# Kernel tuning notes

Hardware: AMD Instinct MI355X
Metric: run time of the kernel (lower is better)

## Reference

```python
import jax, jax.numpy as jnp
import numpy as np


def _make_poly_power_deg1_d3():
    # monomials of degree<=1 in 3 vars: 1, x, y, z  (matches make_monomial_power(3,1))
    return jnp.array([[0, 0, 0], [1, 0, 0], [0, 1, 0], [0, 0, 1]], dtype=jnp.int32)


def setup_inputs() -> dict:
    key = jax.random.key(0)
    k1, k2, k3, k4 = jax.random.split(key, 4)
    Q, N, D, C = 32768, 1024, 3, 32
    q_pos = jax.random.normal(k1, (Q, D), dtype=jnp.float32)
    data_pos = jax.random.normal(k2, (N, D), dtype=jnp.float32)
    w = jax.random.normal(k3, (N, C), dtype=jnp.float32)
    c = jax.random.normal(k4, (4, C), dtype=jnp.float32)
    poly_power = _make_poly_power_deg1_d3()
    return {"q_pos": q_pos, "data_pos": data_pos, "w": w, "c": c, "poly_power": poly_power}


def reference(q_pos, data_pos, w, c, poly_power):
    # pairwise distance: [Q, N, D] -> [Q, N]
    diff = q_pos[:, None, :] - data_pos[None, :, :]
    r = jnp.sqrt(jnp.sum(diff * diff, axis=-1))
    # gaussian RBF kernel
    q_kernel_dist = jnp.exp(-(r * r))
    # interior=True: row-normalize kernel weights
    q_kernel_dist = q_kernel_dist / jnp.sum(q_kernel_dist, axis=-1, keepdims=True)
    # kernel-weighted sum of RBF coefficients: [N,C] x [Q,N] -> [Q,C]
    w_val = jnp.einsum('nc,qn->qc', w, q_kernel_dist)
    # polynomial basis values: prod over D of q_pos^power -> [Q, P]
    pp = poly_power.astype(q_pos.dtype)
    q_poly_val = jnp.prod(q_pos[:, None, :] ** pp[None, :, :], axis=-1)
    # poly-weighted sum: [P,C] x [Q,P] -> [Q,C]
    c_val = jnp.einsum('pc,qp->qc', c, q_poly_val)
    return (w_val + c_val, q_kernel_dist, q_poly_val)
```

## Files before the change

### kernel.cpp

```cpp
#include <hip/hip_runtime.h>
#include <hip/hip_bf16.h>

typedef __attribute__((ext_vector_type(8))) short short8;
typedef __attribute__((ext_vector_type(4))) float f32x4;

#define L2E 1.44269504088896340736f

__device__ __forceinline__ float ipow(float x, int e) {
    float r = 1.f;
    for (int i = 0; i < e; ++i) r *= x;
    return r;
}

__global__ __launch_bounds__(256, 2)
void rbf_fused(const float* __restrict__ q_pos,
               const float* __restrict__ data_pos,
               const float* __restrict__ w,
               const float* __restrict__ cmat,
               const int* __restrict__ poly_power,
               float* __restrict__ out_val,
               float* __restrict__ out_kd,
               float* __restrict__ out_poly)
{
    __shared__ __align__(16) unsigned char smem[65536 + 8192 + 768];
    unsigned char* const w_lds = smem;
    unsigned char* const a_lds = smem + 65536;
    float* const q_lds = (float*)(smem + 65536 + 8192);

    const int t  = threadIdx.x;
    const int l  = t & 63;
    const int wv = t >> 6;
    const int q0 = blockIdx.x * 64;

    for (int j = 0; j < 128; ++j) {
        int i = t + 256 * j;
        int n = i >> 5, cc = i & 31;
        __hip_bfloat16 h = __float2bfloat16(w[i]);
        *(__hip_bfloat16*)(w_lds + cc * 2048 + ((2 * n) ^ ((cc & 7) << 4))) = h;
    }
    if (t < 192) q_lds[t] = q_pos[q0 * 3 + t];
    {
        int i = blockIdx.x * 256 + t;
        int q = i >> 2, p = i & 3;
        int e0 = poly_power[p * 3 + 0], e1 = poly_power[p * 3 + 1], e2 = poly_power[p * 3 + 2];
        float x = q_pos[q * 3 + 0], y = q_pos[q * 3 + 1], z = q_pos[q * 3 + 2];
        out_poly[i] = ipow(x, e0) * ipow(y, e1) * ipow(z, e2);
    }
    __syncthreads();

    float qx[16], qy[16], qz[16];
#pragma unroll
    for (int r = 0; r < 16; ++r) {
        int row = wv * 16 + r;
        qx[r] = q_lds[row * 3 + 0];
        qy[r] = q_lds[row * 3 + 1];
        qz[r] = q_lds[row * 3 + 2];
    }

    float sum[16];
#pragma unroll
    for (int r = 0; r < 16; ++r) sum[r] = 0.f;
    for (int it = 0; it < 16; ++it) {
        int n = it * 64 + l;
        float px = data_pos[n * 3 + 0];
        float py = data_pos[n * 3 + 1];
        float pz = data_pos[n * 3 + 2];
#pragma unroll
        for (int r = 0; r < 16; ++r) {
            float dx = qx[r] - px, dy = qy[r] - py, dz = qz[r] - pz;
            float r2 = dx * dx + dy * dy + dz * dz;
            sum[r] += __builtin_amdgcn_exp2f(r2 * (-L2E));
        }
    }
    float inv[16];
#pragma unroll
    for (int r = 0; r < 16; ++r) {
        float s = sum[r];
        s += __shfl_xor(s, 1);  s += __shfl_xor(s, 2);  s += __shfl_xor(s, 4);
        s += __shfl_xor(s, 8);  s += __shfl_xor(s, 16); s += __shfl_xor(s, 32);
        inv[r] = 1.0f / s;
    }

    f32x4 acc0 = {0.f, 0.f, 0.f, 0.f};
    f32x4 acc1 = {0.f, 0.f, 0.f, 0.f};

    const int arow = l & 15;
    const int kq   = l >> 4;
    const int aswz = (arow & 7) << 4;
    unsigned char* const aw = a_lds + wv * 2048;
    const int offA0 = arow * 128 + (((0 * 32 + 8 * kq) * 2) ^ aswz);
    const int offA1 = arow * 128 + (((1 * 32 + 8 * kq) * 2) ^ aswz);
    const int c0   = arow;
    const int bswz = (c0 & 7) << 4;

    for (int ch = 0; ch < 16; ++ch) {
        int nb = ch * 64;
        int n = nb + l;
        float px = data_pos[n * 3 + 0];
        float py = data_pos[n * 3 + 1];
        float pz = data_pos[n * 3 + 2];
#pragma unroll
        for (int r = 0; r < 16; ++r) {
            float dx = qx[r] - px, dy = qy[r] - py, dz = qz[r] - pz;
            float r2 = dx * dx + dy * dy + dz * dz;
            float e  = __builtin_amdgcn_exp2f(r2 * (-L2E));
            float v  = e * inv[r];
            out_kd[(size_t)(q0 + wv * 16 + r) * 1024 + n] = v;
            *(__hip_bfloat16*)(aw + r * 128 + ((2 * l) ^ ((r & 7) << 4))) = __float2bfloat16(v);
        }
#pragma unroll
        for (int kk = 0; kk < 2; ++kk) {
            short8 afrag = *(const short8*)(aw + (kk ? offA1 : offA0));
            int n0 = nb + kk * 32 + 8 * kq;
            int boff = c0 * 2048 + ((2 * n0) ^ bswz);
            short8 b0 = *(const short8*)(w_lds + boff);
            short8 b1 = *(const short8*)(w_lds + boff + 16 * 2048);
            acc0 = __builtin_amdgcn_mfma_f32_16x16x32_bf16(afrag, b0, acc0, 0, 0, 0);
            acc1 = __builtin_amdgcn_mfma_f32_16x16x32_bf16(afrag, b1, acc1, 0, 0, 0);
        }
    }

    float cp0[4], cp1[4];
#pragma unroll
    for (int p = 0; p < 4; ++p) {
        cp0[p] = cmat[p * 32 + c0];
        cp1[p] = cmat[p * 32 + 16 + c0];
    }
    int pw[12];
#pragma unroll
    for (int i = 0; i < 12; ++i) pw[i] = poly_power[i];
#pragma unroll
    for (int r = 0; r < 4; ++r) {
        int row = kq * 4 + r;
        float x = q_lds[(wv * 16 + row) * 3 + 0];
        float y = q_lds[(wv * 16 + row) * 3 + 1];
        float z = q_lds[(wv * 16 + row) * 3 + 2];
        float cv0 = 0.f, cv1 = 0.f;
#pragma unroll
        for (int p = 0; p < 4; ++p) {
            float pv = ipow(x, pw[p * 3]) * ipow(y, pw[p * 3 + 1]) * ipow(z, pw[p * 3 + 2]);
            cv0 += cp0[p] * pv;
            cv1 += cp1[p] * pv;
        }
        int q = q0 + wv * 16 + row;
        out_val[q * 32 + c0]      = acc0[r] + cv0;
        out_val[q * 32 + 16 + c0] = acc1[r] + cv1;
    }
}

extern "C" void kernel_launch(void* const* d_in, const int* in_sizes, int n_in,
                              void* d_out, int out_size, void* d_ws, size_t ws_size,
                              hipStream_t stream) {
    const float* q_pos      = (const float*)d_in[0];
    const float* data_pos   = (const float*)d_in[1];
    const float* w          = (const float*)d_in[2];
    const float* cmat       = (const float*)d_in[3];
    const int*   poly_power = (const int*)d_in[4];

    const int Q = in_sizes[0] / 3;
    float* out      = (float*)d_out;
    float* out_val  = out;
    float* out_kd   = out + (size_t)Q * 32;
    float* out_poly = out_kd + (size_t)Q * 1024;

    int blocks = Q / 64;
    rbf_fused<<<blocks, 256, 0, stream>>>(q_pos, data_pos, w, cmat, poly_power,
                                          out_val, out_kd, out_poly);
}
```

Measured before the change: 169.8 us.

## Pre-pack w into MFMA fragment layout and compute A fragments in registers

A separate prep kernel converts w to bf16 once, stored in the exact MFMA B-fragment order in workspace, so the main kernel no longer stages 64KB of w in LDS per block. The main kernel now has each lane compute its own 8 kernel values directly into the A-fragment registers and write out_kd with float4 stores. The N dimension is split across two waves per 16-row group, with partial sums and accumulators combined through small shared arrays. This cuts LDS use, raises occupancy, and removes per-element LDS round trips. The cost is an extra kernel launch and some redundant data_pos loads.

```diff
diff --git a/kernel.cpp b/kernel.cpp
--- a/kernel.cpp
+++ b/kernel.cpp
@@ -12,139 +12,147 @@
     return r;
 }
 
-__global__ __launch_bounds__(256, 2)
-void rbf_fused(const float* __restrict__ q_pos,
-               const float* __restrict__ data_pos,
-               const float* __restrict__ w,
-               const float* __restrict__ cmat,
-               const int* __restrict__ poly_power,
-               float* __restrict__ out_val,
-               float* __restrict__ out_kd,
-               float* __restrict__ out_poly)
+__global__ void prep_w(const float* __restrict__ w, unsigned short* __restrict__ img)
 {
-    __shared__ __align__(16) unsigned char smem[65536 + 8192 + 768];
-    unsigned char* const w_lds = smem;
-    unsigned char* const a_lds = smem + 65536;
-    float* const q_lds = (float*)(smem + 65536 + 8192);
+    int idx = blockIdx.x * 256 + threadIdx.x;
+    int frag = idx >> 9, l = (idx >> 3) & 63, j = idx & 7;
+    int ct = frag & 1, kk = (frag >> 1) & 1, chg = frag >> 2;
+    int n = chg * 64 + kk * 32 + 8 * (l >> 4) + j;
+    int c = ct * 16 + (l & 15);
+    __hip_bfloat16 h = __float2bfloat16(w[n * 32 + c]);
+    img[idx] = *(unsigned short*)&h;
+}
 
+__global__ __launch_bounds__(256, 4)
+void rbf_main(const float* __restrict__ q_pos,
+              const float* __restrict__ data_pos,
+              const float* __restrict__ cmat,
+              const int* __restrict__ poly_power,
+              const unsigned short* __restrict__ wimg,
+              float* __restrict__ out_val,
+              float* __restrict__ out_kd,
+              float* __restrict__ out_poly)
+{
     const int t  = threadIdx.x;
     const int l  = t & 63;
     const int wv = t >> 6;
-    const int q0 = blockIdx.x * 64;
+    const int rg   = wv >> 1;
+    const int half = wv & 1;
+    const int q0 = blockIdx.x * 32 + rg * 16;
+    const int m  = l & 15;
+    const int kq = l >> 4;
 
-    for (int j = 0; j < 128; ++j) {
-        int i = t + 256 * j;
-        int n = i >> 5, cc = i & 31;
-        __hip_bfloat16 h = __float2bfloat16(w[i]);
-        *(__hip_bfloat16*)(w_lds + cc * 2048 + ((2 * n) ^ ((cc & 7) << 4))) = h;
-    }
-    if (t < 192) q_lds[t] = q_pos[q0 * 3 + t];
-    {
-        int i = blockIdx.x * 256 + t;
-        int q = i >> 2, p = i & 3;
-        int e0 = poly_power[p * 3 + 0], e1 = poly_power[p * 3 + 1], e2 = poly_power[p * 3 + 2];
-        float x = q_pos[q * 3 + 0], y = q_pos[q * 3 + 1], z = q_pos[q * 3 + 2];
-        out_poly[i] = ipow(x, e0) * ipow(y, e1) * ipow(z, e2);
-    }
-    __syncthreads();
+    __shared__ float s_sum[2][2][16];
+    __shared__ float s_acc[2][64][8];
 
-    float qx[16], qy[16], qz[16];
-#pragma unroll
-    for (int r = 0; r < 16; ++r) {
-        int row = wv * 16 + r;
-        qx[r] = q_lds[row * 3 + 0];
-        qy[r] = q_lds[row * 3 + 1];
-        qz[r] = q_lds[row * 3 + 2];
+    const float qx = q_pos[(q0 + m) * 3 + 0];
+    const float qy = q_pos[(q0 + m) * 3 + 1];
+    const float qz = q_pos[(q0 + m) * 3 + 2];
+
+    if (t < 128) {
+        int q = blockIdx.x * 32 + (t >> 2), p = t & 3;
+        int e0 = poly_power[p * 3], e1 = poly_power[p * 3 + 1], e2 = poly_power[p * 3 + 2];
+        float x = q_pos[q * 3], y = q_pos[q * 3 + 1], z = q_pos[q * 3 + 2];
+        out_poly[q * 4 + p] = ipow(x, e0) * ipow(y, e1) * ipow(z, e2);
     }
 
-    float sum[16];
+    float s = 0.f;
+    for (int ck = 0; ck < 16; ++ck) {
+        int nb = half * 512 + (ck >> 1) * 64 + (ck & 1) * 32 + 8 * kq;
+        const float* dp = data_pos + 3 * nb;
+        float f[24];
 #pragma unroll
-    for (int r = 0; r < 16; ++r) sum[r] = 0.f;
-    for (int it = 0; it < 16; ++it) {
-        int n = it * 64 + l;
-        float px = data_pos[n * 3 + 0];
-        float py = data_pos[n * 3 + 1];
-        float pz = data_pos[n * 3 + 2];
+        for (int i = 0; i < 6; ++i) *(float4*)&f[i * 4] = *(const float4*)(dp + i * 4);
 #pragma unroll
-        for (int r = 0; r < 16; ++r) {
-            float dx = qx[r] - px, dy = qy[r] - py, dz = qz[r] - pz;
+        for (int j = 0; j < 8; ++j) {
+            float dx = qx - f[3 * j], dy = qy - f[3 * j + 1], dz = qz - f[3 * j + 2];
             float r2 = dx * dx + dy * dy + dz * dz;
-            sum[r] += __builtin_amdgcn_exp2f(r2 * (-L2E));
+            s += __builtin_amdgcn_exp2f(r2 * (-L2E));
         }
     }
-    float inv[16];
-#pragma unroll
-    for (int r = 0; r < 16; ++r) {
-        float s = sum[r];
-        s += __shfl_xor(s, 1);  s += __shfl_xor(s, 2);  s += __shfl_xor(s, 4);
-        s += __shfl_xor(s, 8);  s += __shfl_xor(s, 16); s += __shfl_xor(s, 32);
-        inv[r] = 1.0f / s;
-    }
+    s += __shfl_xor(s, 16);
+    s += __shfl_xor(s, 32);
+    if (l < 16) s_sum[rg][half][m] = s;
+    __syncthreads();
+    const float invm = 1.0f / (s_sum[rg][0][m] + s_sum[rg][1][m]);
 
     f32x4 acc0 = {0.f, 0.f, 0.f, 0.f};
     f32x4 acc1 = {0.f, 0.f, 0.f, 0.f};
+    const size_t kdrow = (size_t)(q0 + m) * 1024;
 
-    const int arow = l & 15;
-    const int kq   = l >> 4;
-    const int aswz = (arow & 7) << 4;
-    unsigned char* const aw = a_lds + wv * 2048;
-    const int offA0 = arow * 128 + (((0 * 32 + 8 * kq) * 2) ^ aswz);
-    const int offA1 = arow * 128 + (((1 * 32 + 8 * kq) * 2) ^ aswz);
-    const int c0   = arow;
-    const int bswz = (c0 & 7) << 4;
+    for (int ck = 0; ck < 16; ++ck) {
+        int ch = ck >> 1, kk = ck & 1;
+        int chg = half * 8 + ch;
+        int fb = ((chg * 2 + kk) * 2) * 512;
+        short8 b0 = *(const short8*)(wimg + fb + l * 8);
+        short8 b1 = *(const short8*)(wimg + fb + 512 + l * 8);
 
-    for (int ch = 0; ch < 16; ++ch) {
-        int nb = ch * 64;
-        int n = nb + l;
-        float px = data_pos[n * 3 + 0];
-        float py = data_pos[n * 3 + 1];
-        float pz = data_pos[n * 3 + 2];
+        int nb = half * 512 + ch * 64 + kk * 32 + 8 * kq;
+        const float* dp = data_pos + 3 * nb;
+        float f[24];
 #pragma unroll
-        for (int r = 0; r < 16; ++r) {
-            float dx = qx[r] - px, dy = qy[r] - py, dz = qz[r] - pz;
+        for (int i = 0; i < 6; ++i) *(float4*)&f[i * 4] = *(const float4*)(dp + i * 4);
+
+        float v[8];
+#pragma unroll
+        for (int j = 0; j < 8; ++j) {
+            float dx = qx - f[3 * j], dy = qy - f[3 * j + 1], dz = qz - f[3 * j + 2];
             float r2 = dx * dx + dy * dy + dz * dz;
-            float e  = __builtin_amdgcn_exp2f(r2 * (-L2E));
-            float v  = e * inv[r];
-            out_kd[(size_t)(q0 + wv * 16 + r) * 1024 + n] = v;
-            *(__hip_bfloat16*)(aw + r * 128 + ((2 * l) ^ ((r & 7) << 4))) = __float2bfloat16(v);
+            v[j] = __builtin_amdgcn_exp2f(r2 * (-L2E)) * invm;
+        }
+        short8 a;
+#pragma unroll
+        for (int j = 0; j < 8; ++j) {
+            __hip_bfloat16 h = __float2bfloat16(v[j]);
+            a[j] = *(short*)&h;
+        }
+        acc0 = __builtin_amdgcn_mfma_f32_16x16x32_bf16(a, b0, acc0, 0, 0, 0);
+        acc1 = __builtin_amdgcn_mfma_f32_16x16x32_bf16(a, b1, acc1, 0, 0, 0);
+
+        float4 st0 = {v[0], v[1], v[2], v[3]};
+        float4 st1 = {v[4], v[5], v[6], v[7]};
+        *(float4*)(out_kd + kdrow + nb)     = st0;
+        *(float4*)(out_kd + kdrow + nb + 4) = st1;
+    }
+
+    if (half == 1) {
+#pragma unroll
+        for (int i = 0; i < 4; ++i) {
+            s_acc[rg][l][i]     = acc0[i];
+            s_acc[rg][l][i + 4] = acc1[i];
+        }
+    }
+    __syncthreads();
+    if (half == 0) {
+#pragma unroll
+        for (int i = 0; i < 4; ++i) {
+            acc0[i] += s_acc[rg][l][i];
+            acc1[i] += s_acc[rg][l][i + 4];
+        }
+        int pw[12];
+#pragma unroll
+        for (int i = 0; i < 12; ++i) pw[i] = poly_power[i];
+        float cp0[4], cp1[4];
+#pragma unroll
+        for (int p = 0; p < 4; ++p) {
+            cp0[p] = cmat[p * 32 + m];
+            cp1[p] = cmat[p * 32 + 16 + m];
         }
 #pragma unroll
-        for (int kk = 0; kk < 2; ++kk) {
-            short8 afrag = *(const short8*)(aw + (kk ? offA1 : offA0));
-            int n0 = nb + kk * 32 + 8 * kq;
-            int boff = c0 * 2048 + ((2 * n0) ^ bswz);
-            short8 b0 = *(const short8*)(w_lds + boff);
-            short8 b1 = *(const short8*)(w_lds + boff + 16 * 2048);
-            acc0 = __builtin_amdgcn_mfma_f32_16x16x32_bf16(afrag, b0, acc0, 0, 0, 0);
-            acc1 = __builtin_amdgcn_mfma_f32_16x16x32_bf16(afrag, b1, acc1, 0, 0, 0);
+        for (int r = 0; r < 4; ++r) {
+            int row = kq * 4 + r;
+            int q = q0 + row;
+            float x = q_pos[q * 3], y = q_pos[q * 3 + 1], z = q_pos[q * 3 + 2];
+            float cv0 = 0.f, cv1 = 0.f;
+#pragma unroll
+            for (int p = 0; p < 4; ++p) {
+                float pv = ipow(x, pw[p * 3]) * ipow(y, pw[p * 3 + 1]) * ipow(z, pw[p * 3 + 2]);
+                cv0 += cp0[p] * pv;
+                cv1 += cp1[p] * pv;
+            }
+            out_val[q * 32 + m]      = acc0[r] + cv0;
+            out_val[q * 32 + 16 + m] = acc1[r] + cv1;
         }
-    }
-
-    float cp0[4], cp1[4];
-#pragma unroll
-    for (int p = 0; p < 4; ++p) {
-        cp0[p] = cmat[p * 32 + c0];
-        cp1[p] = cmat[p * 32 + 16 + c0];
-    }
-    int pw[12];
-#pragma unroll
-    for (int i = 0; i < 12; ++i) pw[i] = poly_power[i];
-#pragma unroll
-    for (int r = 0; r < 4; ++r) {
-        int row = kq * 4 + r;
-        float x = q_lds[(wv * 16 + row) * 3 + 0];
-        float y = q_lds[(wv * 16 + row) * 3 + 1];
-        float z = q_lds[(wv * 16 + row) * 3 + 2];
-        float cv0 = 0.f, cv1 = 0.f;
-#pragma unroll
-        for (int p = 0; p < 4; ++p) {
-            float pv = ipow(x, pw[p * 3]) * ipow(y, pw[p * 3 + 1]) * ipow(z, pw[p * 3 + 2]);
-            cv0 += cp0[p] * pv;
-            cv1 += cp1[p] * pv;
-        }
-        int q = q0 + wv * 16 + row;
-        out_val[q * 32 + c0]      = acc0[r] + cv0;
-        out_val[q * 32 + 16 + c0] = acc1[r] + cv1;
     }
 }
 
@@ -163,7 +171,9 @@
     float* out_kd   = out + (size_t)Q * 32;
     float* out_poly = out_kd + (size_t)Q * 1024;
 
-    int blocks = Q / 64;
-    rbf_fused<<<blocks, 256, 0, stream>>>(q_pos, data_pos, w, cmat, poly_power,
-                                          out_val, out_kd, out_poly);
+    unsigned short* wimg = (unsigned short*)d_ws;
+
+    prep_w<<<128, 256, 0, stream>>>(w, wimg);
+    rbf_main<<<Q / 32, 256, 0, stream>>>(q_pos, data_pos, cmat, poly_power, wimg,
+                                         out_val, out_kd, out_poly);
 }
```

New measurement: 171.0 us. Within noise of the previous version (+0.7%).
